# Kernel optimization log

Measured on AMD Instinct MI355X. Metric: run time of the kernel, lower is better.

The kernel has to match this reference:

```python
import jax, jax.numpy as jnp
import numpy as np

N = 16384      # number of nodes
F_IN = 64      # input feature dim
F_OUT = 64     # out_dim


def setup_inputs() -> dict:
    key = jax.random.key(0)
    k1, k2, k3 = jax.random.split(key, 3)
    inp = jax.random.normal(k1, (N, F_IN), dtype=jnp.float32)
    adj = jax.random.uniform(k2, (N, N), dtype=jnp.float32)
    # Dense(out_dim, use_bias=False) kernel, glorot-uniform-ish init
    limit = np.sqrt(6.0 / (F_IN + F_OUT)).astype(np.float32)
    W = jax.random.uniform(k3, (F_IN, F_OUT), dtype=jnp.float32, minval=-limit, maxval=limit)
    b = jnp.zeros((F_OUT,), dtype=jnp.float32)  # gcn_b, zeros init
    return {"input": inp, "adj": adj, "W": W, "b": b}


def reference(input, adj, W, b):
    # x = Dense(x) ; x = adj @ x ; x += b
    h = input @ W                  # [N, F_out]
    out = adj @ h + b              # [N, F_out]
    return out
```

## Files before the change

### kernel.cpp

```cpp
#include <hip/hip_runtime.h>
#include <hip/hip_bf16.h>
#include <stdint.h>

typedef __attribute__((ext_vector_type(4))) float f32x4;
typedef __attribute__((ext_vector_type(8))) __bf16 bf16x8;
typedef __attribute__((ext_vector_type(2))) unsigned int u32x2;
typedef __attribute__((ext_vector_type(4))) unsigned int u32x4;

#define N_NODES 16384
#define F_DIM   64
#define BM      64
#define BK      64

__device__ inline unsigned cvtpk_bf16(float lo, float hi) {
    unsigned r;
    asm("v_cvt_pk_bf16_f32 %0, %1, %2" : "=v"(r) : "v"(lo), "v"(hi));
    return r;
}

__global__ __launch_bounds__(256) void dense_h(const float* __restrict__ inp,
                                               const float* __restrict__ W,
                                               short* __restrict__ hpack) {
    __shared__ float in_lds[64][64];
    __shared__ float wt_lds[64][68];
    const int t = threadIdx.x;
    const int blk = blockIdx.x;

#pragma unroll
    for (int i = 0; i < 4; ++i) {
        int n = i * 256 + t; int row = n >> 4; int c = n & 15;
        f32x4 v = *(const f32x4*)(inp + (size_t)(blk * 64 + row) * 64 + c * 4);
        *(f32x4*)(&in_lds[row][c * 4]) = v;
    }
#pragma unroll
    for (int i = 0; i < 4; ++i) {
        int n = i * 256 + t; int k = n >> 4; int c = n & 15;
        f32x4 v = *(const f32x4*)(W + k * 64 + c * 4);
        wt_lds[c * 4 + 0][k] = v.x; wt_lds[c * 4 + 1][k] = v.y;
        wt_lds[c * 4 + 2][k] = v.z; wt_lds[c * 4 + 3][k] = v.w;
    }
    __syncthreads();

#pragma unroll
    for (int cc = 0; cc < 2; ++cc) {
        int c = cc * 256 + t;
        int kbL = c >> 8; int ct = (c >> 6) & 3; int l = c & 63;
        int f  = ct * 16 + (l & 15);
        int r0 = kbL * 32 + (l >> 4) * 8;
        float acc[8] = {0, 0, 0, 0, 0, 0, 0, 0};
        for (int k = 0; k < 64; k += 4) {
            f32x4 wv = *(const f32x4*)(&wt_lds[f][k]);
#pragma unroll
            for (int j = 0; j < 8; ++j) {
                f32x4 iv = *(const f32x4*)(&in_lds[r0 + j][k]);
                acc[j] += iv.x * wv.x + iv.y * wv.y + iv.z * wv.z + iv.w * wv.w;
            }
        }
        unsigned p0 = cvtpk_bf16(acc[0], acc[1]);
        unsigned p1 = cvtpk_bf16(acc[2], acc[3]);
        unsigned p2 = cvtpk_bf16(acc[4], acc[5]);
        unsigned p3 = cvtpk_bf16(acc[6], acc[7]);
        u32x4 w4 = {p0, p1, p2, p3};
        int kb = blk * 2 + kbL;
        *(u32x4*)(hpack + ((size_t)(kb * 4 + ct) * 64 + l) * 8) = w4;
    }
}

__global__ __launch_bounds__(256, 4) void spmm_adj(const float* __restrict__ adj,
                                                   const short* __restrict__ hp,
                                                   float* __restrict__ out,
                                                   const float* __restrict__ bias) {
    const int rb  = blockIdx.x;
    const int sp  = blockIdx.y;
    const int nsp = gridDim.y;
    const int kspan = N_NODES / nsp;
    const int iters = kspan / BK;
    const int k0    = sp * kspan;
    const int t  = threadIdx.x;
    const int wv = t >> 6;
    const int ln = t & 63;

    __shared__ short At[2][BM * BK];

    const size_t rowbase = (size_t)(rb * BM) * N_NODES;

    auto ldA = [&](int tt, f32x4* rv) {
        size_t base = rowbase + (size_t)(k0 + tt * BK);
#pragma unroll
        for (int i = 0; i < 4; ++i) {
            int n = i * 256 + t; int row = n >> 4; int c = n & 15;
            rv[i] = *(const f32x4*)(adj + base + (size_t)row * N_NODES + c * 4);
        }
    };
    auto stA = [&](int buf, const f32x4* rv) {
#pragma unroll
        for (int i = 0; i < 4; ++i) {
            int n = i * 256 + t; int row = n >> 4; int c = n & 15;
            unsigned lo = cvtpk_bf16(rv[i].x, rv[i].y);
            unsigned hi = cvtpk_bf16(rv[i].z, rv[i].w);
            int byte = row * 128 + ((c * 8) ^ ((row & 7) << 4));
            u32x2 w = {lo, hi};
            *(u32x2*)((char*)At[buf] + byte) = w;
        }
    };

    f32x4 acc[4] = {{0,0,0,0},{0,0,0,0},{0,0,0,0},{0,0,0,0}};
    const int arow  = wv * 16 + (ln & 15);
    const int abase = arow * 128;
    const int axor  = (ln & 7) << 4;
    const int koff  = (ln >> 4) * 16;

    f32x4 rv[4];
    ldA(0, rv);
    stA(0, rv);

    for (int tt = 0; tt < iters; ++tt) {
        const int cur = tt & 1;
        const bool more = (tt + 1 < iters);
        if (more) ldA(tt + 1, rv);
        asm volatile("s_waitcnt lgkmcnt(0)" ::: "memory");
        __builtin_amdgcn_s_barrier();
#pragma unroll
        for (int ks2 = 0; ks2 < 2; ++ks2) {
            bf16x8 a = *(const bf16x8*)((const char*)At[cur] + abase + ((ks2 * 64 + koff) ^ axor));
            const short* hbase = hp + ((size_t)((k0 >> 5) + tt * 2 + ks2) * 4) * 512;
#pragma unroll
            for (int ct = 0; ct < 4; ++ct) {
                bf16x8 b = *(const bf16x8*)(hbase + ct * 512 + ln * 8);
                acc[ct] = __builtin_amdgcn_mfma_f32_16x16x32_bf16(a, b, acc[ct], 0, 0, 0);
            }
        }
        if (more) stA(cur ^ 1, rv);
    }

    float* o = out + (size_t)sp * ((size_t)N_NODES * F_DIM);
    const int orow0 = rb * BM + wv * 16 + (ln >> 4) * 4;
    const int col   = ln & 15;
#pragma unroll
    for (int ct = 0; ct < 4; ++ct) {
#pragma unroll
        for (int j = 0; j < 4; ++j) {
            float v = acc[ct][j];
            if (bias) v += bias[ct * 16 + col];
            o[(size_t)(orow0 + j) * F_DIM + ct * 16 + col] = v;
        }
    }
}

__global__ __launch_bounds__(256) void reduce_add(const float* __restrict__ part,
                                                  const float* __restrict__ bias,
                                                  float* __restrict__ out, int nsp) {
    int g = blockIdx.x * 256 + threadIdx.x;
    f32x4 s = {0, 0, 0, 0};
    for (int i = 0; i < nsp; ++i)
        s += *(const f32x4*)(part + (size_t)i * ((size_t)N_NODES * F_DIM) + (size_t)g * 4);
    f32x4 bv = *(const f32x4*)(bias + ((g * 4) & 63));
    *(f32x4*)(out + (size_t)g * 4) = s + bv;
}

extern "C" void kernel_launch(void* const* d_in, const int* in_sizes, int n_in,
                              void* d_out, int out_size, void* d_ws, size_t ws_size,
                              hipStream_t stream) {
    const float* inp = (const float*)d_in[0];
    const float* adj = (const float*)d_in[1];
    const float* W   = (const float*)d_in[2];
    const float* b   = (const float*)d_in[3];
    float* out = (float*)d_out;

    char*  ws = (char*)d_ws;
    const size_t HP = (size_t)N_NODES * F_DIM * sizeof(short);
    short* hpack = (short*)ws;
    float* partial = (float*)(ws + HP);
    const size_t P1 = (size_t)N_NODES * F_DIM * sizeof(float);

    dense_h<<<N_NODES / 64, 256, 0, stream>>>(inp, W, hpack);

    if (ws_size >= HP + 4 * P1) {
        dim3 g(N_NODES / BM, 4);
        spmm_adj<<<g, 256, 0, stream>>>(adj, hpack, partial, nullptr);
        reduce_add<<<(N_NODES * F_DIM) / 1024, 256, 0, stream>>>(partial, b, out, 4);
    } else if (ws_size >= HP + P1) {
        dim3 g(N_NODES / BM, 1);
        spmm_adj<<<g, 256, 0, stream>>>(adj, hpack, partial, nullptr);
        reduce_add<<<(N_NODES * F_DIM) / 1024, 256, 0, stream>>>(partial, b, out, 1);
    } else {
        dim3 g(N_NODES / BM, 1);
        spmm_adj<<<g, 256, 0, stream>>>(adj, hpack, out, b);
    }
}
```

Baseline: 217.7 us.

## Load adj directly into MFMA registers, drop LDS staging, split K eight ways

The spmm kernel no longer stages the adj tile through shared memory. Each lane now loads the fp32 adj values that match its MFMA A-fragment layout with nontemporal loads, converts them to bf16 in registers, and prefetches both A and B fragments one step ahead with register double buffering, which removes the barriers and LDS traffic. The K split grows from 4 to 8 partial slices, so there are more blocks in flight but more partial-sum traffic for the reduce step. The risks are less coalesced global reads (32-byte segments per lane per row) and higher register pressure.

```diff
diff --git a/kernel.cpp b/kernel.cpp
--- a/kernel.cpp
+++ b/kernel.cpp
@@ -4,18 +4,22 @@
 
 typedef __attribute__((ext_vector_type(4))) float f32x4;
 typedef __attribute__((ext_vector_type(8))) __bf16 bf16x8;
-typedef __attribute__((ext_vector_type(2))) unsigned int u32x2;
 typedef __attribute__((ext_vector_type(4))) unsigned int u32x4;
 
 #define N_NODES 16384
 #define F_DIM   64
-#define BM      64
-#define BK      64
 
 __device__ inline unsigned cvtpk_bf16(float lo, float hi) {
     unsigned r;
     asm("v_cvt_pk_bf16_f32 %0, %1, %2" : "=v"(r) : "v"(lo), "v"(hi));
     return r;
+}
+
+__device__ inline bf16x8 pack8(const f32x4 a, const f32x4 b) {
+    union { u32x4 u; bf16x8 h; } cv;
+    cv.u = (u32x4){cvtpk_bf16(a.x, a.y), cvtpk_bf16(a.z, a.w),
+                   cvtpk_bf16(b.x, b.y), cvtpk_bf16(b.z, b.w)};
+    return cv.h;
 }
 
 __global__ __launch_bounds__(256) void dense_h(const float* __restrict__ inp,
@@ -56,95 +60,91 @@
                 acc[j] += iv.x * wv.x + iv.y * wv.y + iv.z * wv.z + iv.w * wv.w;
             }
         }
-        unsigned p0 = cvtpk_bf16(acc[0], acc[1]);
-        unsigned p1 = cvtpk_bf16(acc[2], acc[3]);
-        unsigned p2 = cvtpk_bf16(acc[4], acc[5]);
-        unsigned p3 = cvtpk_bf16(acc[6], acc[7]);
-        u32x4 w4 = {p0, p1, p2, p3};
+        u32x4 w4 = {cvtpk_bf16(acc[0], acc[1]), cvtpk_bf16(acc[2], acc[3]),
+                    cvtpk_bf16(acc[4], acc[5]), cvtpk_bf16(acc[6], acc[7])};
         int kb = blk * 2 + kbL;
         *(u32x4*)(hpack + ((size_t)(kb * 4 + ct) * 64 + l) * 8) = w4;
     }
 }
 
-__global__ __launch_bounds__(256, 4) void spmm_adj(const float* __restrict__ adj,
-                                                   const short* __restrict__ hp,
-                                                   float* __restrict__ out,
-                                                   const float* __restrict__ bias) {
-    const int rb  = blockIdx.x;
-    const int sp  = blockIdx.y;
-    const int nsp = gridDim.y;
-    const int kspan = N_NODES / nsp;
-    const int iters = kspan / BK;
-    const int k0    = sp * kspan;
+__global__ __launch_bounds__(256) void spmm_adj(const float* __restrict__ adj,
+                                                const short* __restrict__ hp,
+                                                float* __restrict__ out,
+                                                int kspan) {
+    const int rb = blockIdx.x;
+    const int sp = blockIdx.y;
+    const int k0 = sp * kspan;
+    const int iters = kspan >> 6;
     const int t  = threadIdx.x;
     const int wv = t >> 6;
     const int ln = t & 63;
 
-    __shared__ short At[2][BM * BK];
+    const int arow = rb * 64 + wv * 16 + (ln & 15);
+    const int kc   = (ln >> 4) * 8;
 
-    const size_t rowbase = (size_t)(rb * BM) * N_NODES;
+    const float* pA = adj + (size_t)arow * N_NODES + k0 + kc;
+    const short* pB = hp + (size_t)(k0 >> 5) * 2048 + ln * 8;
 
-    auto ldA = [&](int tt, f32x4* rv) {
-        size_t base = rowbase + (size_t)(k0 + tt * BK);
+    auto ldA = [&](int tt, f32x4& x0, f32x4& x1, f32x4& x2, f32x4& x3) {
+        const float* p = pA + (size_t)tt * 64;
+        x0 = __builtin_nontemporal_load((const f32x4*)(p));
+        x1 = __builtin_nontemporal_load((const f32x4*)(p + 4));
+        x2 = __builtin_nontemporal_load((const f32x4*)(p + 32));
+        x3 = __builtin_nontemporal_load((const f32x4*)(p + 36));
+    };
+    auto ldB = [&](int tt, bf16x8* b) {
+        const short* h = pB + (size_t)tt * 4096;
 #pragma unroll
-        for (int i = 0; i < 4; ++i) {
-            int n = i * 256 + t; int row = n >> 4; int c = n & 15;
-            rv[i] = *(const f32x4*)(adj + base + (size_t)row * N_NODES + c * 4);
-        }
-    };
-    auto stA = [&](int buf, const f32x4* rv) {
+        for (int ks2 = 0; ks2 < 2; ++ks2)
 #pragma unroll
-        for (int i = 0; i < 4; ++i) {
-            int n = i * 256 + t; int row = n >> 4; int c = n & 15;
-            unsigned lo = cvtpk_bf16(rv[i].x, rv[i].y);
-            unsigned hi = cvtpk_bf16(rv[i].z, rv[i].w);
-            int byte = row * 128 + ((c * 8) ^ ((row & 7) << 4));
-            u32x2 w = {lo, hi};
-            *(u32x2*)((char*)At[buf] + byte) = w;
-        }
+            for (int ct = 0; ct < 4; ++ct)
+                b[ks2 * 4 + ct] = *(const bf16x8*)(h + ks2 * 2048 + ct * 512);
     };
 
     f32x4 acc[4] = {{0,0,0,0},{0,0,0,0},{0,0,0,0},{0,0,0,0}};
-    const int arow  = wv * 16 + (ln & 15);
-    const int abase = arow * 128;
-    const int axor  = (ln & 7) << 4;
-    const int koff  = (ln >> 4) * 16;
+    f32x4 aC0, aC1, aC2, aC3, aN0, aN1, aN2, aN3;
+    bf16x8 bC[8], bN[8];
 
-    f32x4 rv[4];
-    ldA(0, rv);
-    stA(0, rv);
+    ldB(0, bC);
+    ldA(0, aC0, aC1, aC2, aC3);
 
-    for (int tt = 0; tt < iters; ++tt) {
-        const int cur = tt & 1;
-        const bool more = (tt + 1 < iters);
-        if (more) ldA(tt + 1, rv);
-        asm volatile("s_waitcnt lgkmcnt(0)" ::: "memory");
-        __builtin_amdgcn_s_barrier();
+    for (int tt = 0; tt < iters; tt += 2) {
+        ldB(tt + 1, bN);
+        ldA(tt + 1, aN0, aN1, aN2, aN3);
+        {
+            bf16x8 af0 = pack8(aC0, aC1);
+            bf16x8 af1 = pack8(aC2, aC3);
 #pragma unroll
-        for (int ks2 = 0; ks2 < 2; ++ks2) {
-            bf16x8 a = *(const bf16x8*)((const char*)At[cur] + abase + ((ks2 * 64 + koff) ^ axor));
-            const short* hbase = hp + ((size_t)((k0 >> 5) + tt * 2 + ks2) * 4) * 512;
+            for (int ct = 0; ct < 4; ++ct)
+                acc[ct] = __builtin_amdgcn_mfma_f32_16x16x32_bf16(af0, bC[ct], acc[ct], 0, 0, 0);
 #pragma unroll
-            for (int ct = 0; ct < 4; ++ct) {
-                bf16x8 b = *(const bf16x8*)(hbase + ct * 512 + ln * 8);
-                acc[ct] = __builtin_amdgcn_mfma_f32_16x16x32_bf16(a, b, acc[ct], 0, 0, 0);
-            }
+            for (int ct = 0; ct < 4; ++ct)
+                acc[ct] = __builtin_amdgcn_mfma_f32_16x16x32_bf16(af1, bC[4 + ct], acc[ct], 0, 0, 0);
         }
-        if (more) stA(cur ^ 1, rv);
+        if (tt + 2 < iters) {
+            ldB(tt + 2, bC);
+            ldA(tt + 2, aC0, aC1, aC2, aC3);
+        }
+        {
+            bf16x8 af0 = pack8(aN0, aN1);
+            bf16x8 af1 = pack8(aN2, aN3);
+#pragma unroll
+            for (int ct = 0; ct < 4; ++ct)
+                acc[ct] = __builtin_amdgcn_mfma_f32_16x16x32_bf16(af0, bN[ct], acc[ct], 0, 0, 0);
+#pragma unroll
+            for (int ct = 0; ct < 4; ++ct)
+                acc[ct] = __builtin_amdgcn_mfma_f32_16x16x32_bf16(af1, bN[4 + ct], acc[ct], 0, 0, 0);
+        }
     }
 
     float* o = out + (size_t)sp * ((size_t)N_NODES * F_DIM);
-    const int orow0 = rb * BM + wv * 16 + (ln >> 4) * 4;
+    const int orow0 = rb * 64 + wv * 16 + (ln >> 4) * 4;
     const int col   = ln & 15;
 #pragma unroll
-    for (int ct = 0; ct < 4; ++ct) {
+    for (int ct = 0; ct < 4; ++ct)
 #pragma unroll
-        for (int j = 0; j < 4; ++j) {
-            float v = acc[ct][j];
-            if (bias) v += bias[ct * 16 + col];
-            o[(size_t)(orow0 + j) * F_DIM + ct * 16 + col] = v;
-        }
-    }
+        for (int j = 0; j < 4; ++j)
+            o[(size_t)(orow0 + j) * F_DIM + ct * 16 + col] = acc[ct][j];
 }
 
 __global__ __launch_bounds__(256) void reduce_add(const float* __restrict__ part,
@@ -175,16 +175,17 @@
 
     dense_h<<<N_NODES / 64, 256, 0, stream>>>(inp, W, hpack);
 
-    if (ws_size >= HP + 4 * P1) {
-        dim3 g(N_NODES / BM, 4);
-        spmm_adj<<<g, 256, 0, stream>>>(adj, hpack, partial, nullptr);
-        reduce_add<<<(N_NODES * F_DIM) / 1024, 256, 0, stream>>>(partial, b, out, 4);
+    if (ws_size >= HP + 8 * P1) {
+        dim3 g(N_NODES / 64, 8);
+        spmm_adj<<<g, 256, 0, stream>>>(adj, hpack, partial, N_NODES / 8);
+        reduce_add<<<(N_NODES * F_DIM) / 1024, 256, 0, stream>>>(partial, b, out, 8);
     } else if (ws_size >= HP + P1) {
-        dim3 g(N_NODES / BM, 1);
-        spmm_adj<<<g, 256, 0, stream>>>(adj, hpack, partial, nullptr);
+        dim3 g(N_NODES / 64, 1);
+        spmm_adj<<<g, 256, 0, stream>>>(adj, hpack, partial, N_NODES);
         reduce_add<<<(N_NODES * F_DIM) / 1024, 256, 0, stream>>>(partial, b, out, 1);
     } else {
-        dim3 g(N_NODES / BM, 1);
-        spmm_adj<<<g, 256, 0, stream>>>(adj, hpack, out, b);
+        dim3 g(N_NODES / 64, 1);
+        spmm_adj<<<g, 256, 0, stream>>>(adj, hpack, out, N_NODES);
+        reduce_add<<<(N_NODES * F_DIM) / 1024, 256, 0, stream>>>(out, b, out, 1);
     }
 }
```

New measurement: 343.5 us. 57.8% more time.
